# Kernel optimization log

Measured on AMD Instinct MI355X. Metric: run time of the kernel, lower is better.

Reference implementation:

```python
import jax, jax.numpy as jnp
import numpy as np

# 2nd-order Sobel kernels (kornia get_sobel_kernel2d_2nd_order): d2/dx2, d2/dxdy, d2/dy2
_KXX = np.array([[1., -2., 1.], [2., -4., 2.], [1., -2., 1.]], np.float32)
_KXY = np.array([[-1., 0., 1.], [0., 0., 0.], [1., 0., -1.]], np.float32)
_KERNELS = jnp.asarray(np.stack([_KXX, _KXY, _KXX.T])[:, None])  # (3,1,3,3)


def setup_inputs() -> dict:
    key = jax.random.key(0)
    x = jax.random.normal(key, (16, 3, 1024, 1024), dtype=jnp.float32)
    return {"x": x}


def reference(x):
    scale = 1.0
    B, C, H, W = x.shape
    # spatial_gradient_2nd_order: replicate pad + 3x3 conv per channel
    xp = jnp.pad(x.reshape(B * C, 1, H, W), ((0, 0), (0, 0), (1, 1), (1, 1)), mode='edge')
    g = jax.lax.conv_general_dilated(xp, _KERNELS, (1, 1), 'VALID')  # (B*C, 3, H, W)
    gxx, gxy, gyy = g[:, 0], g[:, 1], g[:, 2]
    # abs determinant of Hessian, clamp
    scores = jnp.abs(gxx * gyy - gxy * gxy) * (scale ** 4)
    scores = jnp.maximum(scores, 1e-6).reshape(B, C, H, W)
    # NMS via 3x3 max-pool (stride 1, SAME): keep only local maxima
    pooled = jax.lax.reduce_window(scores, -jnp.inf, jax.lax.max,
                                   (1, 1, 3, 3), (1, 1, 1, 1), 'SAME')
    scores = jnp.where(scores == pooled, scores, jnp.zeros((), scores.dtype))
    # global max normalization (adaptive_max_pool2d to 1x1)
    smax = jnp.max(scores, axis=(2, 3), keepdims=True)  # (B,C,1,1)
    return scores / smax
```

## Files before the change

### kernel.cpp

```cpp
#include <hip/hip_runtime.h>

#define H 1024
#define W 1024
#define HW (H * W)
#define TROWS 16
#define LROWS 20
#define SLOTF 1024

typedef __attribute__((address_space(3))) float lds_f;
typedef const __attribute__((address_space(1))) float g_f;

__device__ __forceinline__ void gload16(const float* g, float* l) {
    __builtin_amdgcn_global_load_lds((g_f*)g, (lds_f*)l, 16, 0, 0);
}

template<int N>
__device__ __forceinline__ void wait_vm_barrier() {
    asm volatile("s_waitcnt vmcnt(%0)\n\ts_barrier" :: "i"(N) : "memory");
}

__device__ __forceinline__ void stage(const float* px, int row, float* slotbase, int wq, int t) {
    row = row < 0 ? 0 : (row > H - 1 ? H - 1 : row);
    gload16(px + (size_t)row * W + (t << 2), slotbase + wq);
}

__device__ __forceinline__ float score_ref(
    float a00, float a01, float a02,
    float a10, float a11, float a12,
    float a20, float a21, float a22)
{
#pragma clang fp contract(off)
    float gxx = fmaf(-2.0f, a01, a00);
    gxx = gxx + a02;
    gxx = fmaf(2.0f, a10, gxx);
    gxx = fmaf(-4.0f, a11, gxx);
    gxx = fmaf(2.0f, a12, gxx);
    gxx = gxx + a20;
    gxx = fmaf(-2.0f, a21, gxx);
    gxx = gxx + a22;
    float gxy = a02 - a00;
    gxy = gxy + a20;
    gxy = gxy - a22;
    float gyy = fmaf(2.0f, a01, a00);
    gyy = gyy + a02;
    gyy = fmaf(-2.0f, a10, gyy);
    gyy = fmaf(-4.0f, a11, gyy);
    gyy = fmaf(-2.0f, a12, gyy);
    gyy = gyy + a20;
    gyy = fmaf(2.0f, a21, gyy);
    gyy = gyy + a22;

    float p1 = gxx * gyy;
    float p2 = gxy * gxy;
    float det = p1 - p2;
    float s = fabsf(det);
    return s > 1e-6f ? s : 1e-6f;
}

struct Row8 { float a[8]; };

__device__ __forceinline__ Row8 read_win(const float* p, int t)
{
    const int c = t << 2;
    const float2 L  = *(const float2*)(p + (t == 0 ? 0 : c - 2));
    const float4 M  = *(const float4*)(p + c);
    const float2 Rr = *(const float2*)(p + (t == 255 ? 1022 : c + 4));
    Row8 r;
    r.a[0] = L.x;
    r.a[1] = (t == 0) ? L.x : L.y;
    r.a[2] = M.x; r.a[3] = M.y; r.a[4] = M.z; r.a[5] = M.w;
    r.a[6] = (t == 255) ? Rr.y : Rr.x;
    r.a[7] = Rr.y;
    return r;
}

struct S6 { float s[6]; };

__device__ __forceinline__ S6 score_row_exact(const Row8& A, const Row8& B, const Row8& C)
{
    S6 o;
#pragma unroll
    for (int i = 0; i < 6; ++i)
        o.s[i] = score_ref(A.a[i], A.a[i + 1], A.a[i + 2],
                           B.a[i], B.a[i + 1], B.a[i + 2],
                           C.a[i], C.a[i + 1], C.a[i + 2]);
    return o;
}

__global__ __launch_bounds__(256) void hess_score_nms(
    const float* __restrict__ x, float* __restrict__ out,
    unsigned int* __restrict__ pmax)
{
    __shared__ float lds[LROWS * SLOTF];
    const int plane = blockIdx.y;
    const int y0 = blockIdx.x * TROWS;
    const int t = threadIdx.x;
    const int wq = (t >> 6) << 8;
    const float* px = x + (size_t)plane * HW;
    float* po = out + (size_t)plane * HW;

#pragma unroll
    for (int k = 0; k < LROWS; ++k)
        stage(px, y0 - 2 + k, lds + k * SLOTF, wq, t);

    wait_vm_barrier<16>();
    Row8 rm2 = read_win(lds, t);
    Row8 r0  = read_win(lds + SLOTF, t);
    Row8 r1  = read_win(lds + 2 * SLOTF, t);
    Row8 r2  = read_win(lds + 3 * SLOTF, t);

    S6 zero;
#pragma unroll
    for (int i = 0; i < 6; ++i) zero.s[i] = 0.0f;

    S6 sp = zero;
    if (y0 > 0) sp = score_row_exact(rm2, r0, r1);
    S6 sc_ = score_row_exact(r0, r1, r2);

    float smax = 1e-6f;
    for (int r = 0; r < TROWS; ++r) {
        const int sy = y0 + r;
        wait_vm_barrier<15>();

        Row8 r3 = read_win(lds + (r + 4) * SLOTF, t);

        S6 sn = zero;
        if (sy + 1 < H) sn = score_row_exact(r1, r2, r3);

        float m3[6];
#pragma unroll
        for (int k = 0; k < 6; ++k)
            m3[k] = fmaxf(fmaxf(sp.s[k], sc_.s[k]), sn.s[k]);

        float4 o;
        float* ov = (float*)&o;
#pragma unroll
        for (int j = 0; j < 4; ++j) {
            float s = sc_.s[j + 1];
            smax = fmaxf(smax, s);
            float m = fmaxf(fmaxf(m3[j], m3[j + 1]), m3[j + 2]);
            ov[j] = (s == m) ? s : 0.0f;
        }
        *(float4*)(po + (size_t)sy * W + (t << 2)) = o;

        r1 = r2; r2 = r3;
        sp = sc_; sc_ = sn;
    }

#pragma unroll
    for (int off = 32; off > 0; off >>= 1)
        smax = fmaxf(smax, __shfl_down(smax, off));
    if ((t & 63) == 0)
        atomicMax(pmax + plane, __float_as_uint(smax));
}

__global__ __launch_bounds__(256) void hess_scale(
    float* __restrict__ out, const unsigned int* __restrict__ pmax)
{
    const int plane = blockIdx.y;
    const float inv = 1.0f / __uint_as_float(pmax[plane]);
    float4* p = (float4*)(out + (size_t)plane * HW);
    const int idx = blockIdx.x * 256 + threadIdx.x;
#pragma unroll
    for (int k = 0; k < 4; ++k) {
        float4 v = p[idx + (k << 16)];
        v.x *= inv; v.y *= inv; v.z *= inv; v.w *= inv;
        p[idx + (k << 16)] = v;
    }
}

extern "C" void kernel_launch(void* const* d_in, const int* in_sizes, int n_in,
                              void* d_out, int out_size, void* d_ws, size_t ws_size,
                              hipStream_t stream) {
    const float* x = (const float*)d_in[0];
    float* out = (float*)d_out;
    unsigned int* pmax = (unsigned int*)d_ws;
    const int planes = in_sizes[0] / HW;

    hipMemsetAsync(pmax, 0, planes * sizeof(unsigned int), stream);

    dim3 grid1(H / TROWS, planes);
    hess_score_nms<<<grid1, 256, 0, stream>>>(x, out, pmax);

    dim3 grid2(256, planes);
    hess_scale<<<grid2, 256, 0, stream>>>(out, pmax);
}
```

Measured before the change: 444.6 us.

## Replace LDS staging with register ring buffer of direct global row loads

```diff
diff --git a/kernel.cpp b/kernel.cpp
--- a/kernel.cpp
+++ b/kernel.cpp
@@ -3,26 +3,7 @@
 #define H 1024
 #define W 1024
 #define HW (H * W)
-#define TROWS 16
-#define LROWS 20
-#define SLOTF 1024
-
-typedef __attribute__((address_space(3))) float lds_f;
-typedef const __attribute__((address_space(1))) float g_f;
-
-__device__ __forceinline__ void gload16(const float* g, float* l) {
-    __builtin_amdgcn_global_load_lds((g_f*)g, (lds_f*)l, 16, 0, 0);
-}
-
-template<int N>
-__device__ __forceinline__ void wait_vm_barrier() {
-    asm volatile("s_waitcnt vmcnt(%0)\n\ts_barrier" :: "i"(N) : "memory");
-}
-
-__device__ __forceinline__ void stage(const float* px, int row, float* slotbase, int wq, int t) {
-    row = row < 0 ? 0 : (row > H - 1 ? H - 1 : row);
-    gload16(px + (size_t)row * W + (t << 2), slotbase + wq);
-}
+#define STRIP 32
 
 __device__ __forceinline__ float score_ref(
     float a00, float a01, float a02,
@@ -59,12 +40,14 @@
 
 struct Row8 { float a[8]; };
 
-__device__ __forceinline__ Row8 read_win(const float* p, int t)
+__device__ __forceinline__ Row8 load_row8(const float* __restrict__ px, int row, int t)
 {
+    row = row < 0 ? 0 : (row > H - 1 ? H - 1 : row);
+    const float* prow = px + (size_t)row * W;
     const int c = t << 2;
-    const float2 L  = *(const float2*)(p + (t == 0 ? 0 : c - 2));
-    const float4 M  = *(const float4*)(p + c);
-    const float2 Rr = *(const float2*)(p + (t == 255 ? 1022 : c + 4));
+    const float4 M  = *(const float4*)(prow + c);
+    const float2 L  = *(const float2*)(prow + (t == 0 ? 0 : c - 2));
+    const float2 Rr = *(const float2*)(prow + (t == 255 ? 1022 : c + 4));
     Row8 r;
     r.a[0] = L.x;
     r.a[1] = (t == 0) ? L.x : L.y;
@@ -87,64 +70,63 @@
     return o;
 }
 
-__global__ __launch_bounds__(256) void hess_score_nms(
+__global__ __launch_bounds__(256, 4) void hess_score_nms(
     const float* __restrict__ x, float* __restrict__ out,
     unsigned int* __restrict__ pmax)
 {
-    __shared__ float lds[LROWS * SLOTF];
     const int plane = blockIdx.y;
-    const int y0 = blockIdx.x * TROWS;
+    const int y0 = blockIdx.x * STRIP;
     const int t = threadIdx.x;
-    const int wq = (t >> 6) << 8;
     const float* px = x + (size_t)plane * HW;
     float* po = out + (size_t)plane * HW;
 
+    Row8 ring[8];
 #pragma unroll
-    for (int k = 0; k < LROWS; ++k)
-        stage(px, y0 - 2 + k, lds + k * SLOTF, wq, t);
+    for (int k = 0; k < 8; ++k)
+        ring[k] = load_row8(px, y0 - 2 + k, t);
 
-    wait_vm_barrier<16>();
-    Row8 rm2 = read_win(lds, t);
-    Row8 r0  = read_win(lds + SLOTF, t);
-    Row8 r1  = read_win(lds + 2 * SLOTF, t);
-    Row8 r2  = read_win(lds + 3 * SLOTF, t);
+    Row8 r1 = ring[2];
+    Row8 r2 = ring[3];
 
     S6 zero;
 #pragma unroll
     for (int i = 0; i < 6; ++i) zero.s[i] = 0.0f;
 
     S6 sp = zero;
-    if (y0 > 0) sp = score_row_exact(rm2, r0, r1);
-    S6 sc_ = score_row_exact(r0, r1, r2);
+    if (y0 > 0) sp = score_row_exact(ring[0], ring[1], r1);
+    S6 sc_ = score_row_exact(ring[1], r1, r2);
 
     float smax = 1e-6f;
-    for (int r = 0; r < TROWS; ++r) {
-        const int sy = y0 + r;
-        wait_vm_barrier<15>();
+    for (int io = 0; io < STRIP; io += 8) {
+#pragma unroll
+        for (int k = 0; k < 8; ++k) {
+            const int i = io + k;
+            const int sy = y0 + i;
+            Row8 r3 = ring[(i + 4) & 7];
+            ring[i & 7] = load_row8(px, sy + 6, t);
 
-        Row8 r3 = read_win(lds + (r + 4) * SLOTF, t);
+            S6 sn = zero;
+            if (sy + 1 < H) sn = score_row_exact(r1, r2, r3);
 
-        S6 sn = zero;
-        if (sy + 1 < H) sn = score_row_exact(r1, r2, r3);
+            float m3[6];
+#pragma unroll
+            for (int q = 0; q < 6; ++q)
+                m3[q] = fmaxf(fmaxf(sp.s[q], sc_.s[q]), sn.s[q]);
 
-        float m3[6];
+            float4 o;
+            float* ov = (float*)&o;
 #pragma unroll
-        for (int k = 0; k < 6; ++k)
-            m3[k] = fmaxf(fmaxf(sp.s[k], sc_.s[k]), sn.s[k]);
+            for (int j = 0; j < 4; ++j) {
+                float s = sc_.s[j + 1];
+                smax = fmaxf(smax, s);
+                float m = fmaxf(fmaxf(m3[j], m3[j + 1]), m3[j + 2]);
+                ov[j] = (s == m) ? s : 0.0f;
+            }
+            *(float4*)(po + (size_t)sy * W + (t << 2)) = o;
 
-        float4 o;
-        float* ov = (float*)&o;
-#pragma unroll
-        for (int j = 0; j < 4; ++j) {
-            float s = sc_.s[j + 1];
-            smax = fmaxf(smax, s);
-            float m = fmaxf(fmaxf(m3[j], m3[j + 1]), m3[j + 2]);
-            ov[j] = (s == m) ? s : 0.0f;
+            r1 = r2; r2 = r3;
+            sp = sc_; sc_ = sn;
         }
-        *(float4*)(po + (size_t)sy * W + (t << 2)) = o;
-
-        r1 = r2; r2 = r3;
-        sp = sc_; sc_ = sn;
     }
 
 #pragma unroll
@@ -179,7 +161,7 @@
 
     hipMemsetAsync(pmax, 0, planes * sizeof(unsigned int), stream);
 
-    dim3 grid1(H / TROWS, planes);
+    dim3 grid1(H / STRIP, planes);
     hess_score_nms<<<grid1, 256, 0, stream>>>(x, out, pmax);
 
     dim3 grid2(256, planes);
```

Result: faster. 414.3 us (-6.8%).
